# Kernel tuning notes

Measured on AMD Instinct MI355X. Metric: run time of the kernel, lower is better.

The kernel has to match this reference:

```python
import jax, jax.numpy as jnp
import numpy as np

N, NFEAT, NHID, NCLASS, NIDX = 200000, 512, 128, 70, 10000


def normalize_l2(X):
    # row L2-normalize; norm is detached in the original (stop_gradient),
    # inf scale (zero rows) mapped to 0
    rownorm = jax.lax.stop_gradient(jnp.linalg.norm(X, axis=1, keepdims=True))
    scale = jnp.where(rownorm > 0, 1.0 / rownorm, 0.0)
    return X * scale


def setup_inputs() -> dict:
    key = jax.random.key(0)
    ks = jax.random.split(key, 9)
    x = jax.random.normal(ks[0], (N, NFEAT), dtype=jnp.float32)
    simple_features = jax.random.normal(ks[1], (N, NFEAT), dtype=jnp.float32)
    idx = jax.random.randint(ks[2], (NIDX,), 0, N)
    s = 0.05
    W0 = jax.random.normal(ks[3], (NHID, NFEAT), dtype=jnp.float32) * s
    W1 = jax.random.normal(ks[4], (NHID, NFEAT), dtype=jnp.float32) * s
    G1 = jax.random.normal(ks[5], (NHID, NHID), dtype=jnp.float32) * s
    G2 = jax.random.normal(ks[6], (NHID, NHID), dtype=jnp.float32) * s
    GT = jax.random.normal(ks[7], (NHID, 2 * NHID), dtype=jnp.float32) * s
    Wc = jax.random.normal(ks[8], (NCLASS, NHID), dtype=jnp.float32) * s
    return {"x": x, "simple_features": simple_features, "idx": idx,
            "W0": W0, "W1": W1, "G1": G1, "G2": G2, "GT": GT, "Wc": Wc}


def reference(x, simple_features, idx, W0, W1, G1, G2, GT, Wc):
    x = normalize_l2(x)                      # [N, nfeat]
    sf = normalize_l2(simple_features)       # [N, nfeat]
    # dropout/dropout_adj are identity (p=0)
    layer_inner = jax.nn.relu(x @ W0.T)      # [N, nhid]
    lay_simple = jax.nn.relu(sf @ W1.T)      # [N, nhid]
    gate1 = layer_inner @ G1.T               # [N, nhid]
    gate2 = lay_simple @ G2.T                # [N, nhid]
    gate = jax.nn.sigmoid(jnp.concatenate([gate1, gate2], axis=1) @ GT.T)
    fix_inner = (1.0 - gate) * layer_inner + gate * lay_simple
    fix_inner = normalize_l2(fix_inner)
    logits = jax.nn.relu(fix_inner @ Wc.T)   # [N, nclass]
    return jax.nn.log_softmax(logits, axis=-1)[idx]
```

## Files before the change

### kernel.cpp

```cpp
#include <hip/hip_runtime.h>
#include <math.h>

#define NFEAT  512
#define NHID   128
#define NCLASS 70
#define NIDX   10000
#define NTILE  625
#define HELEMS (2u * NIDX * NHID)
#define WIMG_ELEMS (2u * 128 * 512)
#define SMALL_ELEMS 74496u
#define WS_NEED ((size_t)(HELEMS + WIMG_ELEMS + SMALL_ELEMS) * 2)

typedef float  f32x4  __attribute__((ext_vector_type(4)));
typedef __bf16 bf16x8 __attribute__((ext_vector_type(8)));

static __device__ __forceinline__ unsigned short f2bf(float f) {
    unsigned u = __builtin_bit_cast(unsigned, f);
    u += 0x7fffu + ((u >> 16) & 1u);
    return (unsigned short)(u >> 16);
}
static __device__ __forceinline__ float bf2f(unsigned short h) {
    unsigned u = ((unsigned)h) << 16;
    return __builtin_bit_cast(float, u);
}
static __device__ __forceinline__ bf16x8 pack8(float4 a, float4 b) {
    bf16x8 r;
    r[0] = (__bf16)a.x; r[1] = (__bf16)a.y; r[2] = (__bf16)a.z; r[3] = (__bf16)a.w;
    r[4] = (__bf16)b.x; r[5] = (__bf16)b.y; r[6] = (__bf16)b.z; r[7] = (__bf16)b.w;
    return r;
}
static __device__ __forceinline__ bf16x8 pack8s(float4 a, float4 b, float s) {
    bf16x8 r;
    r[0] = (__bf16)(a.x * s); r[1] = (__bf16)(a.y * s); r[2] = (__bf16)(a.z * s); r[3] = (__bf16)(a.w * s);
    r[4] = (__bf16)(b.x * s); r[5] = (__bf16)(b.y * s); r[6] = (__bf16)(b.z * s); r[7] = (__bf16)(b.w * s);
    return r;
}
static __device__ __forceinline__ f32x4 MFMA(bf16x8 a, bf16x8 b, f32x4 c) {
    return __builtin_amdgcn_mfma_f32_16x16x32_bf16(a, b, c, 0, 0, 0);
}
static __device__ __forceinline__ bf16x8 ldsAx(const unsigned short* base, int row, int colb, int rstride) {
    return *(const bf16x8*)((const char*)base + row * rstride + (colb ^ ((row & 7) << 4)));
}
static __device__ __forceinline__ void ldsW1(unsigned short* base, int row, int col, unsigned short v) {
    *(unsigned short*)((char*)base + row * 256 + ((col * 2) ^ ((row & 7) << 4))) = v;
}
static __device__ __forceinline__ float ldsR1(const unsigned short* base, int row, int col) {
    return bf2f(*(const unsigned short*)((const char*)base + row * 256 + ((col * 2) ^ ((row & 7) << 4))));
}

__global__ void prep_weights(const float* __restrict__ W0, const float* __restrict__ W1,
                             const float* __restrict__ G1, const float* __restrict__ G2,
                             const float* __restrict__ GT, const float* __restrict__ Wc,
                             unsigned short* __restrict__ wsWimg,
                             unsigned short* __restrict__ wsSmall) {
    int i = blockIdx.x * 256 + threadIdx.x;
    if (i < 16384) {
        int t = i >> 13;
        int r = i & 8191;
        int n = r >> 6, k8 = r & 63;
        const float* src = (t ? W1 : W0) + (size_t)n * NFEAT + k8 * 8;
        float4 a = ((const float4*)src)[0], b = ((const float4*)src)[1];
        char* dst = (char*)wsWimg + t * 131072 + n * 1024 + ((k8 * 16) ^ ((n & 7) << 4));
        *(bf16x8*)dst = pack8(a, b);
    } else {
        int i4 = i - 16384;
        if (i4 >= 18624) return;
        const float* src; int base4, dstb;
        if      (i4 < 4096)  { src = G1; base4 = 0;     dstb = 0; }
        else if (i4 < 8192)  { src = G2; base4 = 4096;  dstb = 16384; }
        else if (i4 < 16384) { src = GT; base4 = 8192;  dstb = 32768; }
        else                 { src = Wc; base4 = 16384; dstb = 65536; }
        float4 v = ((const float4*)src)[i4 - base4];
        ushort4 o;
        o.x = f2bf(v.x); o.y = f2bf(v.y); o.z = f2bf(v.z); o.w = f2bf(v.w);
        *(ushort4*)(wsSmall + dstb + (size_t)(i4 - base4) * 4) = o;
    }
}

__global__ __launch_bounds__(512) void stageB_ws(
    const float* __restrict__ x, const float* __restrict__ sf,
    const int* __restrict__ idx,
    const unsigned short* __restrict__ wsWimg,
    unsigned short* __restrict__ wsH)
{
    __shared__ __align__(16) unsigned short Wl[65536];
    __shared__ __align__(16) unsigned short Xl[8192];
    __shared__ __align__(16) unsigned short Hl[2048];

    const int tid  = threadIdx.x;
    const int w    = tid >> 6;
    const int lane = tid & 63;
    const int ln   = lane & 15, lg = lane >> 4;
    const int bid  = blockIdx.x;
    const int t    = bid / 125, tb = bid % 125;
    const int tile0 = tb * 5;
    const float* XS = t ? sf : x;
    const f32x4 zero4 = {0.f, 0.f, 0.f, 0.f};

    float4 ga0, ga1, gb0, gb1;
    {
        int r0 = idx[tile0 * 16 + w];
        int r1 = idx[tile0 * 16 + w + 8];
        const float4* p0 = (const float4*)(XS + (size_t)r0 * NFEAT + lane * 8);
        const float4* p1 = (const float4*)(XS + (size_t)r1 * NFEAT + lane * 8);
        ga0 = p0[0]; ga1 = p0[1];
        gb0 = p1[0]; gb1 = p1[1];
    }
    {
        const uint4* src = (const uint4*)((const char*)wsWimg + (size_t)t * 131072);
        uint4* dst = (uint4*)Wl;
        #pragma unroll
        for (int i = 0; i < 16; ++i) dst[tid + i * 512] = src[tid + i * 512];
    }
    auto putX = [&](int m, float4 a, float4 b) {
        float ss = a.x*a.x + a.y*a.y + a.z*a.z + a.w*a.w
                 + b.x*b.x + b.y*b.y + b.z*b.z + b.w*b.w;
        #pragma unroll
        for (int d = 1; d < 64; d <<= 1) ss += __shfl_xor(ss, d);
        float scl = (ss > 0.f) ? (1.f / sqrtf(ss)) : 0.f;
        *(bf16x8*)((char*)Xl + m * 1024 + ((lane * 16) ^ ((m & 7) << 4))) = pack8s(a, b, scl);
    };
    putX(w,     ga0, ga1);
    putX(w + 8, gb0, gb1);
    __syncthreads();

    for (int it = 0; it < 5; ++it) {
        float4 na0, na1, nb0, nb1;
        if (it < 4) {
            int tile = tile0 + it + 1;
            int r0 = idx[tile * 16 + w];
            int r1 = idx[tile * 16 + w + 8];
            const float4* p0 = (const float4*)(XS + (size_t)r0 * NFEAT + lane * 8);
            const float4* p1 = (const float4*)(XS + (size_t)r1 * NFEAT + lane * 8);
            na0 = p0[0]; na1 = p0[1];
            nb0 = p1[0]; nb1 = p1[1];
        }
        f32x4 accE = zero4, accO = zero4;
        #pragma unroll
        for (int kc = 0; kc < 16; ++kc) {
            bf16x8 a = ldsAx(Xl, ln,          kc * 64 + lg * 16, 1024);
            bf16x8 b = ldsAx(Wl, w * 16 + ln, kc * 64 + lg * 16, 1024);
            if (kc & 1) accO = MFMA(a, b, accO); else accE = MFMA(a, b, accE);
        }
        f32x4 acc = accE + accO;
        #pragma unroll
        for (int rg = 0; rg < 4; ++rg)
            ldsW1(Hl, lg * 4 + rg, w * 16 + ln, f2bf(fmaxf(acc[rg], 0.f)));
        __syncthreads();

        if (tid < 256) {
            int tile = tile0 + it;
            ((uint4*)(wsH + ((size_t)t * NIDX + (size_t)tile * 16) * NHID))[tid]
                = ((const uint4*)Hl)[tid];
        }
        if (it < 4) {
            putX(w,     na0, na1);
            putX(w + 8, nb0, nb1);
        }
        __syncthreads();
    }
}

__global__ __launch_bounds__(512) void tailCDE(
    const unsigned short* __restrict__ wsSmall,
    const unsigned short* __restrict__ wsH,
    float* __restrict__ out)
{
    __shared__ __align__(16) unsigned short Hbuf[2][16][NHID];
    __shared__ __align__(16) unsigned short Scr[8704];
    __shared__ float scl2[16];

    unsigned short* G12 = Scr;
    unsigned short* FIX = Scr + 4096;
    float*          LOG = (float*)(Scr + 6144);

    const unsigned short* G1p = wsSmall;
    const unsigned short* G2p = wsSmall + 16384;
    const unsigned short* GTp = wsSmall + 32768;
    const unsigned short* Wcp = wsSmall + 65536;

    const int tid  = threadIdx.x;
    const int bid  = blockIdx.x;
    const int w    = tid >> 6;
    const int lane = tid & 63;
    const int ln   = lane & 15, lg = lane >> 4;
    const int tB = w >> 2, nq = w & 3;
    const f32x4 zero4 = {0.f, 0.f, 0.f, 0.f};

    {
        int tt = tid >> 8, r = tid & 255;
        uint4 v = *(const uint4*)((const char*)wsH
                    + ((size_t)tt * NIDX + (size_t)bid * 16) * 256 + r * 16);
        ((uint4*)&Hbuf[0][0][0])[tid] = v;
    }
    bf16x8 cf[8];
    {
        const unsigned short* Gp = tB ? G2p : G1p;
        #pragma unroll
        for (int kc = 0; kc < 4; ++kc)
            #pragma unroll
            for (int nt = 0; nt < 2; ++nt)
                cf[kc * 2 + nt] = *(const bf16x8*)(Gp + (size_t)(nq * 32 + nt * 16 + ln) * NHID + kc * 32 + lg * 8);
    }
    __syncthreads();

    {
        const unsigned short* Hs = &Hbuf[tB][0][0];
        f32x4 accC[2] = {zero4, zero4};
        #pragma unroll
        for (int kc = 0; kc < 4; ++kc) {
            bf16x8 a = ldsAx(Hs, ln, kc * 64 + lg * 16, 256);
            accC[0] = MFMA(a, cf[kc * 2],     accC[0]);
            accC[1] = MFMA(a, cf[kc * 2 + 1], accC[1]);
        }
        unsigned short* Gd = G12 + tB * 2048;
        #pragma unroll
        for (int nt = 0; nt < 2; ++nt)
            #pragma unroll
            for (int rg = 0; rg < 4; ++rg) {
                int m = lg * 4 + rg;
                ldsW1(Gd, m, nq * 32 + nt * 16 + ln, f2bf(accC[nt][rg]));
            }
    }
    __syncthreads();

    {
        f32x4 accE_ = zero4, accO_ = zero4;
        const int n = w * 16 + ln;
        #pragma unroll
        for (int kc = 0; kc < 8; ++kc) {
            const unsigned short* As = G12 + (kc >> 2) * 2048;
            bf16x8 a = ldsAx(As, ln, (kc & 3) * 64 + lg * 16, 256);
            bf16x8 b = *(const bf16x8*)(GTp + (size_t)n * (2 * NHID) + kc * 32 + lg * 8);
            if (kc & 1) accO_ = MFMA(a, b, accO_); else accE_ = MFMA(a, b, accE_);
        }
        f32x4 accD = accE_ + accO_;
        #pragma unroll
        for (int rg = 0; rg < 4; ++rg) {
            int m = lg * 4 + rg;
            float g  = 1.f / (1.f + __expf(-accD[rg]));
            float h0 = ldsR1(&Hbuf[0][0][0], m, n);
            float h1 = ldsR1(&Hbuf[1][0][0], m, n);
            ldsW1(FIX, m, n, f2bf((1.f - g) * h0 + g * h1));
        }
    }
    __syncthreads();

    if (tid < 256) {
        int r = tid >> 4, sl = tid & 15;
        bf16x8 v = ldsAx(FIX, r, sl * 16, 256);
        float ss = 0.f;
        #pragma unroll
        for (int j = 0; j < 8; ++j) { float f = (float)v[j]; ss += f * f; }
        ss += __shfl_xor(ss, 1); ss += __shfl_xor(ss, 2);
        ss += __shfl_xor(ss, 4); ss += __shfl_xor(ss, 8);
        if (sl == 0) scl2[r] = (ss > 0.f) ? (1.f / sqrtf(ss)) : 0.f;
    }
    __syncthreads();

    if (w < 5) {
        const int cc = w * 16 + ln;
        bf16x8 bfz;
        #pragma unroll
        for (int j = 0; j < 8; ++j) bfz[j] = (__bf16)0.f;
        f32x4 accE = zero4;
        #pragma unroll
        for (int kc = 0; kc < 4; ++kc) {
            bf16x8 a = ldsAx(FIX, ln, kc * 64 + lg * 16, 256);
            bf16x8 b = (cc < NCLASS) ? *(const bf16x8*)(Wcp + (size_t)cc * NHID + kc * 32 + lg * 8) : bfz;
            accE = MFMA(a, b, accE);
        }
        #pragma unroll
        for (int rg = 0; rg < 4; ++rg) {
            int m = lg * 4 + rg;
            float v = fmaxf(accE[rg] * scl2[m], 0.f);
            LOG[m * 80 + cc] = (cc < NCLASS) ? v : -1e30f;
        }
    }
    __syncthreads();

    {
        const int r = tid >> 5, l32 = tid & 31;
        float v0 = LOG[r * 80 + l32];
        float v1 = LOG[r * 80 + 32 + l32];
        float v2 = (l32 < 16) ? LOG[r * 80 + 64 + l32] : -1e30f;
        float mx = fmaxf(fmaxf(v0, v1), v2);
        #pragma unroll
        for (int d = 1; d < 32; d <<= 1) mx = fmaxf(mx, __shfl_xor(mx, d, 32));
        float se = __expf(v0 - mx) + __expf(v1 - mx) + ((l32 < 16) ? __expf(v2 - mx) : 0.f);
        #pragma unroll
        for (int d = 1; d < 32; d <<= 1) se += __shfl_xor(se, d, 32);
        float lz = mx + __logf(se);
        size_t orow = (size_t)bid * 16 + r;
        out[orow * NCLASS + l32] = v0 - lz;
        if (l32 + 32 < NCLASS) out[orow * NCLASS + 32 + l32] = v1 - lz;
        if (l32 + 64 < NCLASS) out[orow * NCLASS + 64 + l32] = v2 - lz;
    }
}

static __device__ __forceinline__ bf16x8 bfragF(const float* p, size_t off) {
    const float4* q = (const float4*)(p + off);
    return pack8(q[0], q[1]);
}
__global__ __launch_bounds__(512) void hyper_fb(
    const float* __restrict__ x, const float* __restrict__ sf,
    const int* __restrict__ idx,
    const float* __restrict__ W0, const float* __restrict__ W1,
    const float* __restrict__ G1, const float* __restrict__ G2,
    const float* __restrict__ GT, const float* __restrict__ Wc,
    float* __restrict__ out)
{
    __shared__ __align__(16) unsigned short Xbuf[2][16][NFEAT];
    __shared__ __align__(16) unsigned short Hbuf[2][16][NHID];
    __shared__ float scl2[16];
    unsigned short* G12 = &Xbuf[0][0][0];
    unsigned short* FIX = &Xbuf[0][0][0] + 4096;
    float*          LOG = (float*)(&Xbuf[0][0][0] + 6144);

    const int tid = threadIdx.x, bid = blockIdx.x;
    const int w = tid >> 6, lane = tid & 63;
    const int ln = lane & 15, lg = lane >> 4;
    const int tB = w >> 2, nq = w & 3;
    const f32x4 zero4 = {0.f, 0.f, 0.f, 0.f};

    {
        char* xb = (char*)&Xbuf[0][0][0];
        #pragma unroll
        for (int j = 0; j < 4; ++j) {
            int p = w * 4 + j, t = p >> 4, m = p & 15;
            int ri = idx[bid * 16 + m];
            const float4* q = (const float4*)((t ? sf : x) + (size_t)ri * NFEAT + lane * 8);
            float4 a = q[0], b = q[1];
            float ss = a.x*a.x + a.y*a.y + a.z*a.z + a.w*a.w
                     + b.x*b.x + b.y*b.y + b.z*b.z + b.w*b.w;
            #pragma unroll
            for (int d = 1; d < 64; d <<= 1) ss += __shfl_xor(ss, d);
            float scl = (ss > 0.f) ? (1.f / sqrtf(ss)) : 0.f;
            int soff = t * 16384 + m * 1024 + ((lane * 16) ^ ((m & 7) << 4));
            *(bf16x8*)(xb + soff) = pack8s(a, b, scl);
        }
    }
    __syncthreads();
    {
        const float* Wp = tB ? W1 : W0;
        f32x4 acc0 = zero4, acc1 = zero4;
        const unsigned short* Xb = (const unsigned short*)((const char*)&Xbuf[0][0][0] + tB * 16384);
        #pragma unroll
        for (int kc = 0; kc < 16; ++kc) {
            bf16x8 a = ldsAx(Xb, ln, kc * 64 + lg * 16, 1024);
            acc0 = MFMA(a, bfragF(Wp, (size_t)(nq * 32 + ln) * NFEAT + kc * 32 + lg * 8), acc0);
            acc1 = MFMA(a, bfragF(Wp, (size_t)(nq * 32 + 16 + ln) * NFEAT + kc * 32 + lg * 8), acc1);
        }
        unsigned short* Hb = &Hbuf[tB][0][0];
        #pragma unroll
        for (int rg = 0; rg < 4; ++rg) {
            int m = lg * 4 + rg;
            ldsW1(Hb, m, nq * 32 + ln,      f2bf(fmaxf(acc0[rg], 0.f)));
            ldsW1(Hb, m, nq * 32 + 16 + ln, f2bf(fmaxf(acc1[rg], 0.f)));
        }
    }
    __syncthreads();
    {
        const float* Gp = tB ? G2 : G1;
        const unsigned short* Hs = &Hbuf[tB][0][0];
        f32x4 accC[2] = {zero4, zero4};
        #pragma unroll
        for (int kc = 0; kc < 4; ++kc) {
            bf16x8 a = ldsAx(Hs, ln, kc * 64 + lg * 16, 256);
            accC[0] = MFMA(a, bfragF(Gp, (size_t)(nq * 32 + ln) * NHID + kc * 32 + lg * 8), accC[0]);
            accC[1] = MFMA(a, bfragF(Gp, (size_t)(nq * 32 + 16 + ln) * NHID + kc * 32 + lg * 8), accC[1]);
        }
        unsigned short* Gd = G12 + tB * 2048;
        #pragma unroll
        for (int nt = 0; nt < 2; ++nt)
            #pragma unroll
            for (int rg = 0; rg < 4; ++rg) {
                int m = lg * 4 + rg;
                ldsW1(Gd, m, nq * 32 + nt * 16 + ln, f2bf(accC[nt][rg]));
            }
    }
    __syncthreads();
    {
        f32x4 accD = zero4;
        const int n = w * 16 + ln;
        #pragma unroll
        for (int kc = 0; kc < 8; ++kc) {
            const unsigned short* As = G12 + (kc >> 2) * 2048;
            bf16x8 a = ldsAx(As, ln, (kc & 3) * 64 + lg * 16, 256);
            accD = MFMA(a, bfragF(GT, (size_t)n * (2 * NHID) + kc * 32 + lg * 8), accD);
        }
        #pragma unroll
        for (int rg = 0; rg < 4; ++rg) {
            int m = lg * 4 + rg;
            float g  = 1.f / (1.f + __expf(-accD[rg]));
            float h0 = ldsR1(&Hbuf[0][0][0], m, n);
            float h1 = ldsR1(&Hbuf[1][0][0], m, n);
            ldsW1(FIX, m, n, f2bf((1.f - g) * h0 + g * h1));
        }
    }
    __syncthreads();
    if (tid < 256) {
        int r = tid >> 4, sl = tid & 15;
        bf16x8 v = ldsAx(FIX, r, sl * 16, 256);
        float ss = 0.f;
        #pragma unroll
        for (int j = 0; j < 8; ++j) { float f = (float)v[j]; ss += f * f; }
        ss += __shfl_xor(ss, 1); ss += __shfl_xor(ss, 2);
        ss += __shfl_xor(ss, 4); ss += __shfl_xor(ss, 8);
        if (sl == 0) scl2[r] = (ss > 0.f) ? (1.f / sqrtf(ss)) : 0.f;
    }
    __syncthreads();
    if (w < 5) {
        const int cc = w * 16 + ln;
        bf16x8 bfz;
        #pragma unroll
        for (int j = 0; j < 8; ++j) bfz[j] = (__bf16)0.f;
        f32x4 accE = zero4;
        #pragma unroll
        for (int kc = 0; kc < 4; ++kc) {
            bf16x8 a = ldsAx(FIX, ln, kc * 64 + lg * 16, 256);
            bf16x8 b = (cc < NCLASS) ? bfragF(Wc, (size_t)cc * NHID + kc * 32 + lg * 8) : bfz;
            accE = MFMA(a, b, accE);
        }
        #pragma unroll
        for (int rg = 0; rg < 4; ++rg) {
            int m = lg * 4 + rg;
            float v = fmaxf(accE[rg] * scl2[m], 0.f);
            LOG[m * 80 + cc] = (cc < NCLASS) ? v : -1e30f;
        }
    }
    __syncthreads();
    {
        const int r = tid >> 5, l32 = tid & 31;
        float v0 = LOG[r * 80 + l32];
        float v1 = LOG[r * 80 + 32 + l32];
        float v2 = (l32 < 16) ? LOG[r * 80 + 64 + l32] : -1e30f;
        float mx = fmaxf(fmaxf(v0, v1), v2);
        #pragma unroll
        for (int d = 1; d < 32; d <<= 1) mx = fmaxf(mx, __shfl_xor(mx, d, 32));
        float se = __expf(v0 - mx) + __expf(v1 - mx) + ((l32 < 16) ? __expf(v2 - mx) : 0.f);
        #pragma unroll
        for (int d = 1; d < 32; d <<= 1) se += __shfl_xor(se, d, 32);
        float lz = mx + __logf(se);
        size_t orow = (size_t)bid * 16 + r;
        out[orow * NCLASS + l32] = v0 - lz;
        if (l32 + 32 < NCLASS) out[orow * NCLASS + 32 + l32] = v1 - lz;
        if (l32 + 64 < NCLASS) out[orow * NCLASS + 64 + l32] = v2 - lz;
    }
}

extern "C" void kernel_launch(void* const* d_in, const int* in_sizes, int n_in,
                              void* d_out, int out_size, void* d_ws, size_t ws_size,
                              hipStream_t stream)
{
    const float* x   = (const float*)d_in[0];
    const float* sf  = (const float*)d_in[1];
    const int*   idx = (const int*)d_in[2];
    const float* W0  = (const float*)d_in[3];
    const float* W1  = (const float*)d_in[4];
    const float* G1  = (const float*)d_in[5];
    const float* G2  = (const float*)d_in[6];
    const float* GT  = (const float*)d_in[7];
    const float* Wc  = (const float*)d_in[8];
    float* out = (float*)d_out;

    if (ws_size >= WS_NEED) {
        unsigned short* wsH     = (unsigned short*)d_ws;
        unsigned short* wsWimg  = wsH + HELEMS;
        unsigned short* wsSmall = wsWimg + WIMG_ELEMS;
        prep_weights<<<dim3(137), dim3(256), 0, stream>>>(W0, W1, G1, G2, GT, Wc, wsWimg, wsSmall);
        stageB_ws<<<dim3(250), dim3(512), 0, stream>>>(x, sf, idx, wsWimg, wsH);
        tailCDE<<<dim3(NTILE), dim3(512), 0, stream>>>(wsSmall, wsH, out);
    } else {
        hyper_fb<<<dim3(NTILE), dim3(512), 0, stream>>>(
            x, sf, idx, W0, W1, G1, G2, GT, Wc, out);
    }
}
```

Measured before the change: 40.83 us.

## Process two row tiles per tail block and keep GT/Wc fragments in registers

The tail kernel now handles two 16-row tiles per workgroup (313 blocks instead of 625). The GT and Wc weight fragments are loaded into registers once and reused for both tiles, instead of being re-read from global memory on each use. This halves the per-tile weight-load and block-launch overhead, at the cost of more LDS and registers per block and fewer blocks to fill the GPU. The softmax was also restructured to use 16 lanes per row, covering both tiles.

Measured after the change: 37.17 us. -9.0%, faster.

```diff
diff --git a/kernel.cpp b/kernel.cpp
--- a/kernel.cpp
+++ b/kernel.cpp
@@ -6,6 +6,7 @@
 #define NCLASS 70
 #define NIDX   10000
 #define NTILE  625
+#define NT2    313
 #define HELEMS (2u * NIDX * NHID)
 #define WIMG_ELEMS (2u * 128 * 512)
 #define SMALL_ELEMS 74496u
@@ -161,18 +162,15 @@
     }
 }
 
-__global__ __launch_bounds__(512) void tailCDE(
+__global__ __launch_bounds__(512) void tailCDE2(
     const unsigned short* __restrict__ wsSmall,
     const unsigned short* __restrict__ wsH,
     float* __restrict__ out)
 {
-    __shared__ __align__(16) unsigned short Hbuf[2][16][NHID];
-    __shared__ __align__(16) unsigned short Scr[8704];
-    __shared__ float scl2[16];
-
-    unsigned short* G12 = Scr;
-    unsigned short* FIX = Scr + 4096;
-    float*          LOG = (float*)(Scr + 6144);
+    __shared__ __align__(16) unsigned short Hbuf[2][2][16][NHID];
+    __shared__ __align__(16) unsigned short G12s[2][2][16][NHID];
+    __shared__ __align__(16) unsigned short FIXs[2][16][NHID];
+    __shared__ float scl2[2][16];
 
     const unsigned short* G1p = wsSmall;
     const unsigned short* G2p = wsSmall + 16384;
@@ -186,12 +184,17 @@
     const int ln   = lane & 15, lg = lane >> 4;
     const int tB = w >> 2, nq = w & 3;
     const f32x4 zero4 = {0.f, 0.f, 0.f, 0.f};
+    const int tile0 = bid * 2;
+    const int tileC1 = (tile0 + 1 < NTILE) ? tile0 + 1 : NTILE - 1;
 
     {
         int tt = tid >> 8, r = tid & 255;
-        uint4 v = *(const uint4*)((const char*)wsH
-                    + ((size_t)tt * NIDX + (size_t)bid * 16) * 256 + r * 16);
-        ((uint4*)&Hbuf[0][0][0])[tid] = v;
+        uint4 v0 = *(const uint4*)((const char*)wsH
+                + ((size_t)tt * NIDX + (size_t)tile0 * 16) * 256 + r * 16);
+        uint4 v1 = *(const uint4*)((const char*)wsH
+                + ((size_t)tt * NIDX + (size_t)tileC1 * 16) * 256 + r * 16);
+        ((uint4*)&Hbuf[0][0][0][0])[tid] = v0;
+        ((uint4*)&Hbuf[1][0][0][0])[tid] = v1;
     }
     bf16x8 cf[8];
     {
@@ -202,10 +205,16 @@
             for (int nt = 0; nt < 2; ++nt)
                 cf[kc * 2 + nt] = *(const bf16x8*)(Gp + (size_t)(nq * 32 + nt * 16 + ln) * NHID + kc * 32 + lg * 8);
     }
-    __syncthreads();
-
-    {
-        const unsigned short* Hs = &Hbuf[tB][0][0];
+    const int nD = w * 16 + ln;
+    bf16x8 gt[8];
+    #pragma unroll
+    for (int kc = 0; kc < 8; ++kc)
+        gt[kc] = *(const bf16x8*)(GTp + (size_t)nD * (2 * NHID) + kc * 32 + lg * 8);
+    __syncthreads();
+
+    #pragma unroll
+    for (int ti = 0; ti < 2; ++ti) {
+        const unsigned short* Hs = &Hbuf[ti][tB][0][0];
         f32x4 accC[2] = {zero4, zero4};
         #pragma unroll
         for (int kc = 0; kc < 4; ++kc) {
@@ -213,7 +222,7 @@
             accC[0] = MFMA(a, cf[kc * 2],     accC[0]);
             accC[1] = MFMA(a, cf[kc * 2 + 1], accC[1]);
         }
-        unsigned short* Gd = G12 + tB * 2048;
+        unsigned short* Gd = &G12s[ti][tB][0][0];
         #pragma unroll
         for (int nt = 0; nt < 2; ++nt)
             #pragma unroll
@@ -222,79 +231,106 @@
                 ldsW1(Gd, m, nq * 32 + nt * 16 + ln, f2bf(accC[nt][rg]));
             }
     }
-    __syncthreads();
-
-    {
-        f32x4 accE_ = zero4, accO_ = zero4;
-        const int n = w * 16 + ln;
+    const int ccE = w * 16 + ln;
+    const int ccl = (ccE < NCLASS) ? ccE : 0;
+    bf16x8 wcf[4];
+    #pragma unroll
+    for (int kc = 0; kc < 4; ++kc)
+        wcf[kc] = *(const bf16x8*)(Wcp + (size_t)ccl * NHID + kc * 32 + lg * 8);
+    __syncthreads();
+
+    #pragma unroll
+    for (int ti = 0; ti < 2; ++ti) {
+        f32x4 aE = zero4, aO = zero4;
         #pragma unroll
         for (int kc = 0; kc < 8; ++kc) {
-            const unsigned short* As = G12 + (kc >> 2) * 2048;
+            const unsigned short* As = &G12s[ti][kc >> 2][0][0];
             bf16x8 a = ldsAx(As, ln, (kc & 3) * 64 + lg * 16, 256);
-            bf16x8 b = *(const bf16x8*)(GTp + (size_t)n * (2 * NHID) + kc * 32 + lg * 8);
-            if (kc & 1) accO_ = MFMA(a, b, accO_); else accE_ = MFMA(a, b, accE_);
-        }
-        f32x4 accD = accE_ + accO_;
+            if (kc & 1) aO = MFMA(a, gt[kc], aO); else aE = MFMA(a, gt[kc], aE);
+        }
+        f32x4 accD = aE + aO;
         #pragma unroll
         for (int rg = 0; rg < 4; ++rg) {
             int m = lg * 4 + rg;
             float g  = 1.f / (1.f + __expf(-accD[rg]));
-            float h0 = ldsR1(&Hbuf[0][0][0], m, n);
-            float h1 = ldsR1(&Hbuf[1][0][0], m, n);
-            ldsW1(FIX, m, n, f2bf((1.f - g) * h0 + g * h1));
-        }
-    }
-    __syncthreads();
-
-    if (tid < 256) {
-        int r = tid >> 4, sl = tid & 15;
-        bf16x8 v = ldsAx(FIX, r, sl * 16, 256);
+            float h0 = ldsR1(&Hbuf[ti][0][0][0], m, nD);
+            float h1 = ldsR1(&Hbuf[ti][1][0][0], m, nD);
+            ldsW1(&FIXs[ti][0][0], m, nD, f2bf((1.f - g) * h0 + g * h1));
+        }
+    }
+    __syncthreads();
+
+    {
+        int rr = tid >> 4, sl = tid & 15;
+        int ti = rr >> 4, r = rr & 15;
+        bf16x8 v = ldsAx(&FIXs[ti][0][0], r, sl * 16, 256);
         float ss = 0.f;
         #pragma unroll
         for (int j = 0; j < 8; ++j) { float f = (float)v[j]; ss += f * f; }
         ss += __shfl_xor(ss, 1); ss += __shfl_xor(ss, 2);
         ss += __shfl_xor(ss, 4); ss += __shfl_xor(ss, 8);
-        if (sl == 0) scl2[r] = (ss > 0.f) ? (1.f / sqrtf(ss)) : 0.f;
+        if (sl == 0) scl2[ti][r] = (ss > 0.f) ? (1.f / sqrtf(ss)) : 0.f;
     }
     __syncthreads();
 
     if (w < 5) {
-        const int cc = w * 16 + ln;
+        const bool live = (ccE < NCLASS);
         bf16x8 bfz;
         #pragma unroll
         for (int j = 0; j < 8; ++j) bfz[j] = (__bf16)0.f;
-        f32x4 accE = zero4;
-        #pragma unroll
-        for (int kc = 0; kc < 4; ++kc) {
-            bf16x8 a = ldsAx(FIX, ln, kc * 64 + lg * 16, 256);
-            bf16x8 b = (cc < NCLASS) ? *(const bf16x8*)(Wcp + (size_t)cc * NHID + kc * 32 + lg * 8) : bfz;
-            accE = MFMA(a, b, accE);
-        }
-        #pragma unroll
-        for (int rg = 0; rg < 4; ++rg) {
-            int m = lg * 4 + rg;
-            float v = fmaxf(accE[rg] * scl2[m], 0.f);
-            LOG[m * 80 + cc] = (cc < NCLASS) ? v : -1e30f;
-        }
-    }
-    __syncthreads();
-
-    {
-        const int r = tid >> 5, l32 = tid & 31;
-        float v0 = LOG[r * 80 + l32];
-        float v1 = LOG[r * 80 + 32 + l32];
-        float v2 = (l32 < 16) ? LOG[r * 80 + 64 + l32] : -1e30f;
-        float mx = fmaxf(fmaxf(v0, v1), v2);
-        #pragma unroll
-        for (int d = 1; d < 32; d <<= 1) mx = fmaxf(mx, __shfl_xor(mx, d, 32));
-        float se = __expf(v0 - mx) + __expf(v1 - mx) + ((l32 < 16) ? __expf(v2 - mx) : 0.f);
-        #pragma unroll
-        for (int d = 1; d < 32; d <<= 1) se += __shfl_xor(se, d, 32);
+        #pragma unroll
+        for (int ti = 0; ti < 2; ++ti) {
+            f32x4 accE = zero4;
+            #pragma unroll
+            for (int kc = 0; kc < 4; ++kc) {
+                bf16x8 a = ldsAx(&FIXs[ti][0][0], ln, kc * 64 + lg * 16, 256);
+                accE = MFMA(a, live ? wcf[kc] : bfz, accE);
+            }
+            if (live) {
+                float* LO = (float*)((char*)&G12s[0][0][0][0] + ti * 8192);
+                #pragma unroll
+                for (int rg = 0; rg < 4; ++rg) {
+                    int m = lg * 4 + rg;
+                    LO[m * 80 + ccE] = fmaxf(accE[rg] * scl2[ti][m], 0.f);
+                }
+            }
+        }
+    }
+    __syncthreads();
+
+    {
+        int rr = tid >> 4, l16 = tid & 15;
+        int ti = rr >> 4, r = rr & 15;
+        const float* LO = (const float*)((const char*)&G12s[0][0][0][0] + ti * 8192) + r * 80;
+        float v[5];
+        #pragma unroll
+        for (int j = 0; j < 5; ++j) {
+            int c = l16 + j * 16;
+            v[j] = (c < NCLASS) ? LO[c] : -1e30f;
+        }
+        float mx = v[0];
+        #pragma unroll
+        for (int j = 1; j < 5; ++j) mx = fmaxf(mx, v[j]);
+        mx = fmaxf(mx, __shfl_xor(mx, 1)); mx = fmaxf(mx, __shfl_xor(mx, 2));
+        mx = fmaxf(mx, __shfl_xor(mx, 4)); mx = fmaxf(mx, __shfl_xor(mx, 8));
+        float se = 0.f;
+        #pragma unroll
+        for (int j = 0; j < 5; ++j) {
+            int c = l16 + j * 16;
+            if (c < NCLASS) se += __expf(v[j] - mx);
+        }
+        se += __shfl_xor(se, 1); se += __shfl_xor(se, 2);
+        se += __shfl_xor(se, 4); se += __shfl_xor(se, 8);
         float lz = mx + __logf(se);
-        size_t orow = (size_t)bid * 16 + r;
-        out[orow * NCLASS + l32] = v0 - lz;
-        if (l32 + 32 < NCLASS) out[orow * NCLASS + 32 + l32] = v1 - lz;
-        if (l32 + 64 < NCLASS) out[orow * NCLASS + 64 + l32] = v2 - lz;
+        int tile = tile0 + ti;
+        if (tile < NTILE) {
+            size_t orow = (size_t)tile * 16 + r;
+            #pragma unroll
+            for (int j = 0; j < 5; ++j) {
+                int c = l16 + j * 16;
+                if (c < NCLASS) out[orow * NCLASS + c] = v[j] - lz;
+            }
+        }
     }
 }
 
@@ -470,7 +506,7 @@
         unsigned short* wsSmall = wsWimg + WIMG_ELEMS;
         prep_weights<<<dim3(137), dim3(256), 0, stream>>>(W0, W1, G1, G2, GT, Wc, wsWimg, wsSmall);
         stageB_ws<<<dim3(250), dim3(512), 0, stream>>>(x, sf, idx, wsWimg, wsH);
-        tailCDE<<<dim3(NTILE), dim3(512), 0, stream>>>(wsSmall, wsH, out);
+        tailCDE2<<<dim3(NT2), dim3(512), 0, stream>>>(wsSmall, wsH, out);
     } else {
         hyper_fb<<<dim3(NTILE), dim3(512), 0, stream>>>(
             x, sf, idx, W0, W1, G1, G2, GT, Wc, out);
```
